# Kernel optimization log

Hardware: AMD Instinct MI355X
Metric: run time of the kernel (lower is better)

Reference implementation:

```python
import jax, jax.numpy as jnp
import numpy as np

NX, DX, H, DO = 8192, 8, 1024, 1


def setup_inputs() -> dict:
    key = jax.random.key(0)
    ks = jax.random.split(key, 7)
    s1 = 1.0 / np.sqrt(DX)  # torch Linear default init bound
    s2 = 1.0 / np.sqrt(H)
    x = jax.random.normal(ks[0], (NX, DX), jnp.float32)
    W1 = jax.random.uniform(ks[1], (H, DX), jnp.float32, -s1, s1)
    b1 = jax.random.uniform(ks[2], (H,), jnp.float32, -s1, s1)
    W2 = jax.random.uniform(ks[3], (H, H), jnp.float32, -s2, s2)
    b2 = jax.random.uniform(ks[4], (H,), jnp.float32, -s2, s2)
    W3 = jax.random.uniform(ks[5], (DO, H), jnp.float32, -s2, s2)
    b3 = jax.random.uniform(ks[6], (DO,), jnp.float32, -s2, s2)
    return {"x": x, "W1": W1, "b1": b1, "W2": W2, "b2": b2, "W3": W3, "b3": b3}


def reference(x, W1, b1, W2, b2, W3, b3):
    # Forward: Linear -> Tanh -> Linear -> Tanh -> Linear
    z1 = jnp.tanh(x @ W1.T + b1)          # [nx, h]
    z2 = jnp.tanh(z1 @ W2.T + b2)         # [nx, h]
    y = z2 @ W3.T + b3                    # [nx, out]

    # DerivTanh(h) = 4/(e^-h + e^h)^2 = sech^2(h) = 1 - tanh(h)^2
    d1 = 1.0 - z1 * z1                    # [nx, h]
    d2 = 1.0 - z2 * z2                    # [nx, h]

    # Vectorized analytic Jacobian (original loops over each input dim k):
    # tmp_k = d2 * (W2 @ (d1 * W1[:, k]))  then  dydx_k = W3 @ tmp_k
    J = d1[:, :, None] * W1[None, :, :]                    # [nx, h, dx]
    J = d2[:, :, None] * jnp.einsum('ij,njk->nik', W2, J)  # [nx, h, dx]
    dydx = jnp.einsum('oj,njk->nok', W3, J)                # [nx, out, dx]
    # Match original list-of-dx ordering: dydx[k] has shape [nx, out]
    dydx = jnp.transpose(dydx, (2, 0, 1))                  # [dx, nx, out]
    return y, dydx
```

## Files before the change

kernel.cpp:

```cpp
#include <hip/hip_runtime.h>
#include <stdint.h>

#define NXS 8192
#define HS  1024

typedef __attribute__((ext_vector_type(8))) short short8;
typedef __attribute__((ext_vector_type(4))) float f32x4;

__device__ __forceinline__ float bf2f(uint32_t b) {
    union { uint32_t u; float f; } c; c.u = b << 16; return c.f;
}
__device__ __forceinline__ uint16_t f2bf(float f) {
    union { float f; uint32_t u; } c; c.f = f;
    return (uint16_t)((c.u + 0x7fffu + ((c.u >> 16) & 1u)) >> 16);
}
__device__ __forceinline__ void async_cp16(const void* g, void* l) {
    __builtin_amdgcn_global_load_lds(
        (const __attribute__((address_space(1))) void*)g,
        (__attribute__((address_space(3))) void*)l,
        16, 0, 0);
}

__global__ __launch_bounds__(256) void k01(
    const float* __restrict__ x, const float* __restrict__ W1,
    const float* __restrict__ b1, const float* __restrict__ W2,
    const float* __restrict__ b3, uint16_t* __restrict__ Z1,
    uint16_t* __restrict__ Bp1, uint16_t* __restrict__ Bp2,
    uint16_t* __restrict__ W1T, float* __restrict__ out)
{
    __shared__ float xs[8][8];
    const int b = blockIdx.x, t = threadIdx.x;
    if (b < 1024) {
        const int n0 = b * 8;
        if (t < 64) xs[t >> 3][t & 7] = x[n0 * 8 + t];
        const int j = t * 4;
        float w[4][8];
#pragma unroll
        for (int c = 0; c < 4; ++c) {
            float4 w0 = *(const float4*)(W1 + (j + c) * 8);
            float4 w1 = *(const float4*)(W1 + (j + c) * 8 + 4);
            w[c][0] = w0.x; w[c][1] = w0.y; w[c][2] = w0.z; w[c][3] = w0.w;
            w[c][4] = w1.x; w[c][5] = w1.y; w[c][6] = w1.z; w[c][7] = w1.w;
        }
        float4 bb = *(const float4*)(b1 + j);
        const float bv[4] = {bb.x, bb.y, bb.z, bb.w};
        __syncthreads();
#pragma unroll
        for (int s = 0; s < 8; ++s) {
            ushort4 o;
            uint16_t* op = (uint16_t*)&o;
#pragma unroll
            for (int c = 0; c < 4; ++c) {
                float sum = bv[c];
#pragma unroll
                for (int k = 0; k < 8; ++k) sum += xs[s][k] * w[c][k];
                op[c] = f2bf(tanhf(sum));
            }
            *(ushort4*)(Z1 + (size_t)(n0 + s) * HS + j) = o;
        }
    } else if (b < 1536) {
        const int tid = (b - 1024) * 256 + t;
        const int l = tid & 63, c = (tid >> 6) & 31, g = tid >> 11;
        const int lr = l & 15, lq = l >> 4;
        const float* src = W2 + (size_t)(g * 16 + lr) * HS + c * 32 + lq * 8;
        float4 a0 = *(const float4*)src;
        float4 a1 = *(const float4*)(src + 4);
        uint16_t o[8];
        o[0] = f2bf(a0.x); o[1] = f2bf(a0.y); o[2] = f2bf(a0.z); o[3] = f2bf(a0.w);
        o[4] = f2bf(a1.x); o[5] = f2bf(a1.y); o[6] = f2bf(a1.z); o[7] = f2bf(a1.w);
        *(ushort4*)(Bp1 + (size_t)tid * 8)     = *(ushort4*)&o[0];
        *(ushort4*)(Bp1 + (size_t)tid * 8 + 4) = *(ushort4*)&o[4];
    } else if (b < 2048) {
        const int tid = (b - 1536) * 256 + t;
        const int l = tid & 63, c = (tid >> 6) & 31, g = tid >> 11;
        const int lr = l & 15, lq = l >> 4;
        uint16_t o[8];
#pragma unroll
        for (int j2 = 0; j2 < 8; ++j2)
            o[j2] = f2bf(W2[(size_t)(c * 32 + lq * 8 + j2) * HS + g * 16 + lr]);
        *(ushort4*)(Bp2 + (size_t)tid * 8)     = *(ushort4*)&o[0];
        *(ushort4*)(Bp2 + (size_t)tid * 8 + 4) = *(ushort4*)&o[4];
    } else if (b < 2336) {
        const int idx = (b - 2048) * 256 + t;
        out[idx] = (idx < NXS) ? b3[0] : 0.f;
    } else {
        const int idx = (b - 2336) * 256 + t;
        const int r = idx >> 10, cc = idx & 1023;
        W1T[idx] = (r < 8) ? f2bf(W1[cc * 8 + r]) : (uint16_t)0;
    }
}

template <int MODE>
__global__ __launch_bounds__(256, 4) void gemm_k(
    const uint16_t* __restrict__ A, const uint16_t* __restrict__ Bp,
    const float* __restrict__ bias, const float* __restrict__ W3,
    uint16_t* __restrict__ Out, float* __restrict__ yOut,
    const uint16_t* __restrict__ Z1, const uint16_t* __restrict__ W1T,
    float* __restrict__ dOut)
{
    __shared__ __attribute__((aligned(16))) uint16_t smem[12288];
    const int t = threadIdx.x;
    const int wave = t >> 6, lane = t & 63;
    const int lq = lane >> 4, lr = lane & 15;
    const int rowBase = blockIdx.x * 64;
    const int colBase = blockIdx.y * 128;

    const int rA = t >> 2, qA = (t & 3) ^ (rA & 3);
    const uint16_t* gA = A + (size_t)(rowBase + rA) * HS + qA * 8;

    const uint16_t* pB0 = Bp + ((size_t)(colBase >> 4) + wave * 2) * 16384 + (size_t)lane * 8;
    const uint16_t* pB1 = pB0 + 16384;

    f32x4 acc[4][2] = {};

    async_cp16(gA, (char*)smem + t * 16);
    short8 b0 = *(const short8*)pB0;
    short8 b1 = *(const short8*)pB1;
    __syncthreads();

    int buf = 0;
    for (int c = 0; c < 32; ++c, buf ^= 1) {
        short8 b0n = b0, b1n = b1;
        if (c < 31) {
            async_cp16(gA + (c + 1) * 32, (char*)smem + (buf ^ 1) * 4096 + t * 16);
            b0n = *(const short8*)(pB0 + (c + 1) * 512);
            b1n = *(const short8*)(pB1 + (c + 1) * 512);
        }
        const short* pA = (const short*)smem + buf * 2048;
        short8 af[4];
#pragma unroll
        for (int ti = 0; ti < 4; ++ti) {
            int ar = ti * 16 + lr;
            af[ti] = *(const short8*)(pA + ar * 32 + ((lq ^ (ar & 3)) << 3));
        }
#pragma unroll
        for (int ti = 0; ti < 4; ++ti) {
            acc[ti][0] = __builtin_amdgcn_mfma_f32_16x16x32_bf16(af[ti], b0, acc[ti][0], 0, 0, 0);
            acc[ti][1] = __builtin_amdgcn_mfma_f32_16x16x32_bf16(af[ti], b1, acc[ti][1], 0, 0, 0);
        }
        __syncthreads();
        b0 = b0n; b1 = b1n;
    }

    if (MODE == 0) {
        float cB[2], cW[2]; int cCol[2];
#pragma unroll
        for (int tj = 0; tj < 2; ++tj) {
            cCol[tj] = colBase + wave * 32 + tj * 16 + lr;
            cB[tj] = bias[cCol[tj]];
            cW[tj] = W3[cCol[tj]];
        }
#pragma unroll
        for (int ti = 0; ti < 4; ++ti) {
#pragma unroll
            for (int r = 0; r < 4; ++r) {
                int row = rowBase + ti * 16 + lq * 4 + r;
                float ys = 0.f;
#pragma unroll
                for (int tj = 0; tj < 2; ++tj) {
                    float z2 = tanhf(acc[ti][tj][r] + cB[tj]);
                    ys += z2 * cW[tj];
                    Out[(size_t)row * HS + cCol[tj]] = f2bf((1.f - z2 * z2) * cW[tj]);
                }
                ys += __shfl_xor(ys, 1); ys += __shfl_xor(ys, 2);
                ys += __shfl_xor(ys, 4); ys += __shfl_xor(ys, 8);
                if (lr == 0) atomicAdd(&yOut[row], ys);
            }
        }
    } else {
#pragma unroll
        for (int ti = 0; ti < 4; ++ti)
#pragma unroll
            for (int r = 0; r < 4; ++r) {
                int rowl = ti * 16 + lq * 4 + r;
                const size_t zrow = (size_t)(rowBase + rowl) * HS + colBase;
#pragma unroll
                for (int tj = 0; tj < 2; ++tj) {
                    int coll = wave * 32 + tj * 16 + lr;
                    float z1 = bf2f(Z1[zrow + coll]);
                    smem[rowl * 136 + coll] =
                        f2bf(acc[ti][tj][r] * (1.f - z1 * z1));
                }
            }
        __syncthreads();
        f32x4 dd = {};
#pragma unroll
        for (int kb = 0; kb < 4; ++kb) {
            short8 aF = *(const short8*)(smem + (wave * 16 + lr) * 136
                                         + kb * 32 + lq * 8);
            short8 bF = *(const short8*)(W1T + lr * HS + colBase
                                         + kb * 32 + lq * 8);
            dd = __builtin_amdgcn_mfma_f32_16x16x32_bf16(aF, bF, dd, 0, 0, 0);
        }
        if (lr < 8) {
            int row = rowBase + wave * 16 + lq * 4;
#pragma unroll
            for (int rg = 0; rg < 4; ++rg)
                atomicAdd(&dOut[(size_t)lr * NXS + row + rg], dd[rg]);
        }
    }
}

extern "C" void kernel_launch(void* const* d_in, const int* in_sizes, int n_in,
                              void* d_out, int out_size, void* d_ws, size_t ws_size,
                              hipStream_t stream) {
    (void)in_sizes; (void)n_in; (void)out_size; (void)ws_size;
    const float* x  = (const float*)d_in[0];
    const float* W1 = (const float*)d_in[1];
    const float* b1 = (const float*)d_in[2];
    const float* W2 = (const float*)d_in[3];
    const float* b2 = (const float*)d_in[4];
    const float* W3 = (const float*)d_in[5];
    const float* b3 = (const float*)d_in[6];
    float* out = (float*)d_out;

    char* ws = (char*)d_ws;
    uint16_t* Z1  = (uint16_t*)(ws);
    uint16_t* V   = (uint16_t*)(ws + (size_t)16 * 1024 * 1024);
    uint16_t* Bp1 = (uint16_t*)(ws + (size_t)32 * 1024 * 1024);
    uint16_t* Bp2 = (uint16_t*)(ws + (size_t)34 * 1024 * 1024);
    uint16_t* W1T = (uint16_t*)(ws + (size_t)36 * 1024 * 1024);

    k01<<<2400, 256, 0, stream>>>(x, W1, b1, W2, b3, Z1, Bp1, Bp2, W1T, out);
    gemm_k<0><<<dim3(NXS / 64, HS / 128), 256, 0, stream>>>(
        Z1, Bp1, b2, W3, V, out, nullptr, nullptr, nullptr);
    gemm_k<1><<<dim3(NXS / 64, HS / 128), 256, 0, stream>>>(
        V, Bp2, nullptr, nullptr, nullptr, nullptr, Z1, W1T, out + NXS);
}
```

Baseline: 138.5 us.

## Enlarge GEMM block tile to 128x128 with 2x2 wave grid and K=64 steps

```diff
diff --git a/kernel.cpp b/kernel.cpp
--- a/kernel.cpp
+++ b/kernel.cpp
@@ -91,62 +91,95 @@
 }
 
 template <int MODE>
-__global__ __launch_bounds__(256, 4) void gemm_k(
+__global__ __launch_bounds__(256, 2) void gemm_k(
     const uint16_t* __restrict__ A, const uint16_t* __restrict__ Bp,
     const float* __restrict__ bias, const float* __restrict__ W3,
     uint16_t* __restrict__ Out, float* __restrict__ yOut,
     const uint16_t* __restrict__ Z1, const uint16_t* __restrict__ W1T,
     float* __restrict__ dOut)
 {
-    __shared__ __attribute__((aligned(16))) uint16_t smem[12288];
+    constexpr int SMEM_U16 = (MODE == 1) ? 17408 : 16384;
+    __shared__ __attribute__((aligned(16))) uint16_t smem[SMEM_U16];
     const int t = threadIdx.x;
     const int wave = t >> 6, lane = t & 63;
     const int lq = lane >> 4, lr = lane & 15;
-    const int rowBase = blockIdx.x * 64;
+    const int wr = wave >> 1, wc = wave & 1;
+    const int rowBase = blockIdx.x * 128;
     const int colBase = blockIdx.y * 128;
 
-    const int rA = t >> 2, qA = (t & 3) ^ (rA & 3);
-    const uint16_t* gA = A + (size_t)(rowBase + rA) * HS + qA * 8;
-
-    const uint16_t* pB0 = Bp + ((size_t)(colBase >> 4) + wave * 2) * 16384 + (size_t)lane * 8;
-    const uint16_t* pB1 = pB0 + 16384;
-
-    f32x4 acc[4][2] = {};
-
-    async_cp16(gA, (char*)smem + t * 16);
-    short8 b0 = *(const short8*)pB0;
-    short8 b1 = *(const short8*)pB1;
+    const uint16_t* gA[4];
+#pragma unroll
+    for (int i = 0; i < 4; ++i) {
+        int s = t + i * 256;
+        int rA = s >> 3, qA = (s & 7) ^ (rA & 7);
+        gA[i] = A + (size_t)(rowBase + rA) * HS + qA * 8;
+    }
+
+    const uint16_t* pB[4];
+#pragma unroll
+    for (int tj = 0; tj < 4; ++tj)
+        pB[tj] = Bp + ((size_t)(colBase >> 4) + wc * 4 + tj) * 16384
+                    + (size_t)lane * 8;
+
+    f32x4 acc[4][4] = {};
+
+#pragma unroll
+    for (int i = 0; i < 4; ++i)
+        async_cp16(gA[i], (char*)smem + t * 16 + i * 4096);
+    short8 bc[4][2];
+#pragma unroll
+    for (int tj = 0; tj < 4; ++tj) {
+        bc[tj][0] = *(const short8*)(pB[tj]);
+        bc[tj][1] = *(const short8*)(pB[tj] + 512);
+    }
     __syncthreads();
 
     int buf = 0;
-    for (int c = 0; c < 32; ++c, buf ^= 1) {
-        short8 b0n = b0, b1n = b1;
-        if (c < 31) {
-            async_cp16(gA + (c + 1) * 32, (char*)smem + (buf ^ 1) * 4096 + t * 16);
-            b0n = *(const short8*)(pB0 + (c + 1) * 512);
-            b1n = *(const short8*)(pB1 + (c + 1) * 512);
-        }
-        const short* pA = (const short*)smem + buf * 2048;
-        short8 af[4];
-#pragma unroll
-        for (int ti = 0; ti < 4; ++ti) {
-            int ar = ti * 16 + lr;
-            af[ti] = *(const short8*)(pA + ar * 32 + ((lq ^ (ar & 3)) << 3));
-        }
-#pragma unroll
-        for (int ti = 0; ti < 4; ++ti) {
-            acc[ti][0] = __builtin_amdgcn_mfma_f32_16x16x32_bf16(af[ti], b0, acc[ti][0], 0, 0, 0);
-            acc[ti][1] = __builtin_amdgcn_mfma_f32_16x16x32_bf16(af[ti], b1, acc[ti][1], 0, 0, 0);
+    for (int c = 0; c < 16; ++c) {
+        short8 bn[4][2];
+        if (c < 15) {
+#pragma unroll
+            for (int i = 0; i < 4; ++i)
+                async_cp16(gA[i] + (c + 1) * 64,
+                           (char*)smem + (buf ^ 1) * 16384 + t * 16 + i * 4096);
+#pragma unroll
+            for (int tj = 0; tj < 4; ++tj) {
+                bn[tj][0] = *(const short8*)(pB[tj] + (c + 1) * 1024);
+                bn[tj][1] = *(const short8*)(pB[tj] + (c + 1) * 1024 + 512);
+            }
+        }
+        const uint16_t* pA = smem + buf * 8192;
+#pragma unroll
+        for (int kk = 0; kk < 2; ++kk) {
+            short8 af[4];
+#pragma unroll
+            for (int ti = 0; ti < 4; ++ti) {
+                int ar = wr * 64 + ti * 16 + lr;
+                af[ti] = *(const short8*)(pA + ar * 64
+                          + ((((kk << 2) + lq) ^ (ar & 7)) << 3));
+            }
+#pragma unroll
+            for (int ti = 0; ti < 4; ++ti)
+#pragma unroll
+                for (int tj = 0; tj < 4; ++tj)
+                    acc[ti][tj] = __builtin_amdgcn_mfma_f32_16x16x32_bf16(
+                        af[ti], bc[tj][kk], acc[ti][tj], 0, 0, 0);
         }
         __syncthreads();
-        b0 = b0n; b1 = b1n;
+        if (c < 15) {
+#pragma unroll
+            for (int tj = 0; tj < 4; ++tj) {
+                bc[tj][0] = bn[tj][0]; bc[tj][1] = bn[tj][1];
+            }
+        }
+        buf ^= 1;
     }
 
     if (MODE == 0) {
-        float cB[2], cW[2]; int cCol[2];
-#pragma unroll
-        for (int tj = 0; tj < 2; ++tj) {
-            cCol[tj] = colBase + wave * 32 + tj * 16 + lr;
+        float cB[4], cW[4]; int cCol[4];
+#pragma unroll
+        for (int tj = 0; tj < 4; ++tj) {
+            cCol[tj] = colBase + wc * 64 + tj * 16 + lr;
             cB[tj] = bias[cCol[tj]];
             cW[tj] = W3[cCol[tj]];
         }
@@ -154,10 +187,10 @@
         for (int ti = 0; ti < 4; ++ti) {
 #pragma unroll
             for (int r = 0; r < 4; ++r) {
-                int row = rowBase + ti * 16 + lq * 4 + r;
+                int row = rowBase + wr * 64 + ti * 16 + lq * 4 + r;
                 float ys = 0.f;
 #pragma unroll
-                for (int tj = 0; tj < 2; ++tj) {
+                for (int tj = 0; tj < 4; ++tj) {
                     float z2 = tanhf(acc[ti][tj][r] + cB[tj]);
                     ys += z2 * cW[tj];
                     Out[(size_t)row * HS + cCol[tj]] = f2bf((1.f - z2 * z2) * cW[tj]);
@@ -172,31 +205,36 @@
         for (int ti = 0; ti < 4; ++ti)
 #pragma unroll
             for (int r = 0; r < 4; ++r) {
-                int rowl = ti * 16 + lq * 4 + r;
+                int rowl = wr * 64 + ti * 16 + lq * 4 + r;
                 const size_t zrow = (size_t)(rowBase + rowl) * HS + colBase;
 #pragma unroll
-                for (int tj = 0; tj < 2; ++tj) {
-                    int coll = wave * 32 + tj * 16 + lr;
+                for (int tj = 0; tj < 4; ++tj) {
+                    int coll = wc * 64 + tj * 16 + lr;
                     float z1 = bf2f(Z1[zrow + coll]);
                     smem[rowl * 136 + coll] =
                         f2bf(acc[ti][tj][r] * (1.f - z1 * z1));
                 }
             }
         __syncthreads();
-        f32x4 dd = {};
-#pragma unroll
-        for (int kb = 0; kb < 4; ++kb) {
-            short8 aF = *(const short8*)(smem + (wave * 16 + lr) * 136
-                                         + kb * 32 + lq * 8);
-            short8 bF = *(const short8*)(W1T + lr * HS + colBase
-                                         + kb * 32 + lq * 8);
-            dd = __builtin_amdgcn_mfma_f32_16x16x32_bf16(aF, bF, dd, 0, 0, 0);
-        }
+        f32x4 dd[2] = {};
+#pragma unroll
+        for (int h = 0; h < 2; ++h)
+#pragma unroll
+            for (int kb = 0; kb < 4; ++kb) {
+                short8 aF = *(const short8*)(smem + (wave * 32 + h * 16 + lr) * 136
+                                             + kb * 32 + lq * 8);
+                short8 bF = *(const short8*)(W1T + (size_t)lr * HS + colBase
+                                             + kb * 32 + lq * 8);
+                dd[h] = __builtin_amdgcn_mfma_f32_16x16x32_bf16(aF, bF, dd[h], 0, 0, 0);
+            }
         if (lr < 8) {
-            int row = rowBase + wave * 16 + lq * 4;
-#pragma unroll
-            for (int rg = 0; rg < 4; ++rg)
-                atomicAdd(&dOut[(size_t)lr * NXS + row + rg], dd[rg]);
+#pragma unroll
+            for (int h = 0; h < 2; ++h) {
+                int row = rowBase + wave * 32 + h * 16 + lq * 4;
+#pragma unroll
+                for (int rg = 0; rg < 4; ++rg)
+                    atomicAdd(&dOut[(size_t)lr * NXS + row + rg], dd[h][rg]);
+            }
         }
     }
 }
@@ -222,8 +260,8 @@
     uint16_t* W1T = (uint16_t*)(ws + (size_t)36 * 1024 * 1024);
 
     k01<<<2400, 256, 0, stream>>>(x, W1, b1, W2, b3, Z1, Bp1, Bp2, W1T, out);
-    gemm_k<0><<<dim3(NXS / 64, HS / 128), 256, 0, stream>>>(
+    gemm_k<0><<<dim3(NXS / 128, HS / 128), 256, 0, stream>>>(
         Z1, Bp1, b2, W3, V, out, nullptr, nullptr, nullptr);
-    gemm_k<1><<<dim3(NXS / 64, HS / 128), 256, 0, stream>>>(
+    gemm_k<1><<<dim3(NXS / 128, HS / 128), 256, 0, stream>>>(
         V, Bp2, nullptr, nullptr, nullptr, nullptr, Z1, W1T, out + NXS);
 }
```

Result: no change. 138.5 us (-0.0%).
